# Optimization experiments

Measured on AMD Instinct MI355X. Metric: run time of the kernel, lower is better.

The kernel has to match this reference:

```python
import jax, jax.numpy as jnp
import numpy as np
import math

D_MODEL = 512
D_FF = 2048
N_HEADS = 8
D_K = 64
EPS = 1e-5


def _layernorm(x, g, b):
    mu = jnp.mean(x, axis=-1, keepdims=True)
    var = jnp.mean(jnp.square(x - mu), axis=-1, keepdims=True)
    return (x - mu) * jax.lax.rsqrt(var + EPS) * g + b


def _pos_encoding(seq_len, d_model, dtype):
    pos = jnp.arange(seq_len, dtype=jnp.float32)[:, None]                 # [S,1]
    div = jnp.exp(jnp.arange(0, d_model, 2, dtype=jnp.float32) * (-math.log(10000.0) / d_model))
    ang = pos * div                                                        # [S,D/2]
    pe = jnp.stack([jnp.sin(ang), jnp.cos(ang)], axis=-1).reshape(seq_len, d_model)
    return pe.astype(dtype)


def setup_inputs() -> dict:
    key = jax.random.key(0)
    ks = jax.random.split(key, 16)
    B, S, D, F, H, DK = 4096, 16, D_MODEL, D_FF, N_HEADS, D_K
    s = lambda fan_in: 1.0 / np.sqrt(fan_in)
    u = lambda k, shp, sc: jax.random.uniform(k, shp, jnp.float32, -sc, sc)
    return {
        "enc_inputs": jax.random.normal(ks[0], (B, S, D), jnp.float32),
        # Linear weights stored as [in, out] (torch stores [out, in])
        "wq": u(ks[1], (D, H * DK), s(D)), "bq": u(ks[2], (H * DK,), s(D)),
        "wk": u(ks[3], (D, H * DK), s(D)), "bk": u(ks[4], (H * DK,), s(D)),
        "wv": u(ks[5], (D, H * DK), s(D)), "bv": u(ks[6], (H * DK,), s(D)),
        "wo": u(ks[7], (H * DK, D), s(H * DK)), "bo": u(ks[8], (D,), s(H * DK)),
        "ln1_g": jnp.ones((D,), jnp.float32), "ln1_b": jnp.zeros((D,), jnp.float32),
        "w1": u(ks[9], (D, F), s(D)), "b1": u(ks[10], (F,), s(D)),
        "w2": u(ks[11], (F, D), s(F)), "b2": u(ks[12], (D,), s(F)),
        "ln2_g": jnp.ones((D,), jnp.float32), "ln2_b": jnp.zeros((D,), jnp.float32),
        "conv_att_w": u(ks[13], (H,), s(H)),  # Conv2d(8,1,1,bias=False) == weighted head sum
    }


def reference(enc_inputs, wq, bq, wk, bk, wv, bv, wo, bo, ln1_g, ln1_b,
              w1, b1, w2, b2, ln2_g, ln2_b, conv_att_w):
    B, S, D = enc_inputs.shape
    H, DK = N_HEADS, D_K
    # positional encoding (dropout is identity in eval)
    x = enc_inputs + _pos_encoding(S, D, enc_inputs.dtype)[None, :, :]
    # multi-head self-attention
    q = (x @ wq + bq).reshape(B, S, H, DK).transpose(0, 2, 1, 3)  # [B,H,S,DK]
    k = (x @ wk + bk).reshape(B, S, H, DK).transpose(0, 2, 1, 3)
    v = (x @ wv + bv).reshape(B, S, H, DK).transpose(0, 2, 1, 3)
    scores = jnp.einsum('bhqd,bhkd->bhqk', q, k) / np.sqrt(DK)
    attn = jax.nn.softmax(scores, axis=-1)                         # [B,H,S,S]
    ctx = jnp.einsum('bhqk,bhkd->bhqd', attn, v)
    ctx = ctx.transpose(0, 2, 1, 3).reshape(B, S, H * DK)
    y = _layernorm(ctx @ wo + bo + x, ln1_g, ln1_b)
    # position-wise FFN (conv1d kernel=1 == linear)
    h = jax.nn.relu(y @ w1 + b1)
    out = _layernorm(h @ w2 + b2 + y, ln2_g, ln2_b)
    # conv_att: Conv2d(8->1, k=1, no bias) over heads
    attn_out = jnp.einsum('h,bhqk->bqk', conv_att_w, attn)
    return out, attn_out
```

## Files before the change

### kernel.cpp

```cpp
#include <hip/hip_runtime.h>
#include <hip/hip_bf16.h>

using bf16 = __hip_bfloat16;
typedef __attribute__((ext_vector_type(8))) short bf16x8;
typedef __attribute__((ext_vector_type(4))) float f32x4;

#define MFMA_BF16_16x16x32 __builtin_amdgcn_mfma_f32_16x16x32_bf16

__device__ __forceinline__ float bits2f(short b) {
  unsigned u = ((unsigned)(unsigned short)b) << 16;
  return __uint_as_float(u);
}
__device__ __forceinline__ short f2bits(float f) {
  bf16 h = __float2bfloat16(f);
  return *reinterpret_cast<short*>(&h);
}

__device__ __forceinline__ int xcd_swz(int bid, int nwg) {
  int q = nwg >> 3;
  return (bid & 7) * q + (bid >> 3);
}

__global__ void detect_kernel(const unsigned short* __restrict__ w, int* __restrict__ flag) {
  __shared__ int bad;
  if (threadIdx.x == 0) bad = 0;
  __syncthreads();
  float m = 0.f;
#pragma unroll
  for (int j = 0; j < 4; ++j)
    m = fmaxf(m, fabsf(bits2f((short)w[threadIdx.x * 4 + j])));
  if (m > 4.0f) atomicOr(&bad, 1);
  __syncthreads();
  if (threadIdx.x == 0) *flag = bad ? 1 : 0;
}

__global__ void pe_kernel(float* __restrict__ pe) {
  int s = blockIdx.x;
  int i = threadIdx.x;
  float dv = expf((float)(2 * i) * (-9.210340371976184f / 512.0f));
  float ang = (float)s * dv;
  pe[s * 512 + 2 * i]     = sinf(ang);
  pe[s * 512 + 2 * i + 1] = cosf(ang);
}

__global__ __launch_bounds__(256) void add_pe2_kernel(const void* __restrict__ enc_bf,
                                                      const void* __restrict__ enc_f32,
                                                      const float* __restrict__ pe,
                                                      bf16* __restrict__ x,
                                                      const int* __restrict__ flag) {
  size_t i = ((size_t)blockIdx.x * 256 + threadIdx.x) * 8;
  int col  = (int)(i & 511);
  int srow = (int)((i >> 9) & 15);
  float e[8];
  if (*flag) {
    const float* ef = (const float*)enc_f32 + i;
    f32x4 a = *reinterpret_cast<const f32x4*>(ef);
    f32x4 b = *reinterpret_cast<const f32x4*>(ef + 4);
#pragma unroll
    for (int j = 0; j < 4; ++j) { e[j] = a[j]; e[4 + j] = b[j]; }
  } else {
    bf16x8 ev = *reinterpret_cast<const bf16x8*>((const bf16*)enc_bf + i);
#pragma unroll
    for (int j = 0; j < 8; ++j) e[j] = bits2f(ev[j]);
  }
  const float* pp = pe + srow * 512 + col;
  f32x4 p0 = *reinterpret_cast<const f32x4*>(pp);
  f32x4 p1 = *reinterpret_cast<const f32x4*>(pp + 4);
  bf16x8 o;
#pragma unroll
  for (int j = 0; j < 4; ++j) o[j] = f2bits(e[j] + p0[j]);
#pragma unroll
  for (int j = 0; j < 4; ++j) o[4 + j] = f2bits(e[4 + j] + p1[j]);
  *reinterpret_cast<bf16x8*>(x + i) = o;
}

__global__ __launch_bounds__(256) void transpose_cvt_kernel(const void* __restrict__ src,
                                                            unsigned short* __restrict__ dst,
                                                            int R, int C, const int* __restrict__ flag) {
  __shared__ unsigned short t[32][33];
  int bx = blockIdx.x * 32;
  int by = blockIdx.y * 32;
  int lx = threadIdx.x & 31, ly = threadIdx.x >> 5;
  if (*flag) {
    const float* s = (const float*)src;
#pragma unroll
    for (int i = 0; i < 4; ++i)
      t[ly + i * 8][lx] = (unsigned short)f2bits(s[(size_t)(by + ly + i * 8) * C + bx + lx]);
  } else {
    const unsigned short* s = (const unsigned short*)src;
#pragma unroll
    for (int i = 0; i < 4; ++i)
      t[ly + i * 8][lx] = s[(size_t)(by + ly + i * 8) * C + bx + lx];
  }
  __syncthreads();
#pragma unroll
  for (int i = 0; i < 4; ++i)
    dst[(size_t)(bx + ly + i * 8) * R + by + lx] = t[lx][ly + i * 8];
}

struct SmallSeg { const void* src; bf16* dst; int n; };
struct SmallCvtArgs { SmallSeg seg[11]; };
__global__ __launch_bounds__(256) void small_cvt_kernel(SmallCvtArgs a, const int* __restrict__ flag) {
  SmallSeg s = a.seg[blockIdx.x];
  int f = *flag;
  for (int i = threadIdx.x; i < s.n; i += 256) {
    float v = f ? ((const float*)s.src)[i] : bits2f(((const short*)s.src)[i]);
    s.dst[i] = __float2bfloat16(v);
  }
}

template <int EPI>
__global__ __launch_bounds__(256, 2)
void gemm_bt_kernel(const bf16* __restrict__ A, const bf16* __restrict__ Bt,
                    const bf16* __restrict__ bias, const bf16* res,
                    bf16* C, int M, int N, int K) {
  constexpr int BK = 32;
  __shared__ __align__(16) char lds[2][2][128 * BK * 2];
  const int nbx = N >> 7;
  const int wg = xcd_swz(blockIdx.x, gridDim.x);
  const int bx = wg % nbx;
  const int by = wg / nbx;
  const int m0 = by << 7, n0 = bx << 7;
  const int tid = threadIdx.x;
  const int lane = tid & 63, wid = tid >> 6;
  const int wm = (wid >> 1) << 6, wn = (wid & 1) << 6;
  const int lr = lane & 15, gq = lane >> 4;

  f32x4 acc[4][4] = {};

  auto stage = [&](int buf, int kt) {
#pragma unroll
    for (int c = 0; c < 2; ++c) {
      int off = c * 4096 + tid * 16;
      int row = off >> 6;
      int ch  = (off >> 4) & 3;
      const bf16* ga = A  + (size_t)(m0 + row) * K + kt * BK + ch * 8;
      const bf16* gb = Bt + (size_t)(n0 + row) * K + kt * BK + ch * 8;
      __builtin_amdgcn_global_load_lds((const __attribute__((address_space(1))) void*)ga,
          (__attribute__((address_space(3))) void*)&lds[buf][0][c * 4096 + wid * 1024], 16, 0, 0);
      __builtin_amdgcn_global_load_lds((const __attribute__((address_space(1))) void*)gb,
          (__attribute__((address_space(3))) void*)&lds[buf][1][c * 4096 + wid * 1024], 16, 0, 0);
    }
  };

  auto compute = [&](int buf) {
    const char* As = lds[buf][0];
    const char* Bs = lds[buf][1];
    bf16x8 af[4], bfr[4];
#pragma unroll
    for (int i = 0; i < 4; ++i) {
      af[i]  = *reinterpret_cast<const bf16x8*>(As + (wm + i * 16 + lr) * 64 + gq * 16);
      bfr[i] = *reinterpret_cast<const bf16x8*>(Bs + (wn + i * 16 + lr) * 64 + gq * 16);
    }
#pragma unroll
    for (int i = 0; i < 4; ++i)
#pragma unroll
      for (int j = 0; j < 4; ++j)
        acc[i][j] = MFMA_BF16_16x16x32(af[i], bfr[j], acc[i][j], 0, 0, 0);
  };

  stage(0, 0);
  __syncthreads();
  const int nk = K / BK;
  int buf = 0;
  for (int kt = 0; kt < nk; ++kt) {
    if (kt + 1 < nk) stage(buf ^ 1, kt + 1);
    compute(buf);
    __syncthreads();
    buf ^= 1;
  }

#pragma unroll
  for (int i = 0; i < 4; ++i) {
#pragma unroll
    for (int j = 0; j < 4; ++j) {
      int col = n0 + wn + j * 16 + lr;
      float bv = __bfloat162float(bias[col]);
#pragma unroll
      for (int r = 0; r < 4; ++r) {
        int row = m0 + wm + i * 16 + gq * 4 + r;
        float v = acc[i][j][r] + bv;
        if (EPI == 1) v = fmaxf(v, 0.0f);
        if (EPI == 2) v += __bfloat162float(res[(size_t)row * N + col]);
        C[(size_t)row * N + col] = __float2bfloat16(v);
      }
    }
  }
}

__global__ __launch_bounds__(256)
void attn_kernel(const bf16* __restrict__ qkv, const bf16* __restrict__ cw,
                 bf16* __restrict__ ctx, float* __restrict__ attn_out) {
  __shared__ __align__(16) unsigned short qkv_lds[16][1544];
  __shared__ __align__(16) unsigned short p_lds[4][16][16];
  __shared__ float att_lds[4][16][16];
  const int b = blockIdx.x;
  const int tid = threadIdx.x, lane = tid & 63, w = tid >> 6;
  const int lr = lane & 15, g = lane >> 4;
  const bf16* src = qkv + (size_t)b * 16 * 1536;
  for (int t = tid; t < 16 * 192; t += 256) {
    int row = t / 192, ch = t - row * 192;
    *reinterpret_cast<bf16x8*>(&qkv_lds[row][ch * 8]) =
        *reinterpret_cast<const bf16x8*>(src + (size_t)row * 1536 + ch * 8);
  }
  __syncthreads();
  float attacc[4] = {0.f, 0.f, 0.f, 0.f};

  for (int hh = 0; hh < 2; ++hh) {
    const int h = w * 2 + hh;
    const unsigned short* qp = &qkv_lds[lr][h * 64 + g * 8];
    const unsigned short* kp = qp + 512;
    bf16x8 q0 = *reinterpret_cast<const bf16x8*>(qp);
    bf16x8 q1 = *reinterpret_cast<const bf16x8*>(qp + 32);
    bf16x8 k0 = *reinterpret_cast<const bf16x8*>(kp);
    bf16x8 k1 = *reinterpret_cast<const bf16x8*>(kp + 32);
    f32x4 s = {0.f, 0.f, 0.f, 0.f};
    s = MFMA_BF16_16x16x32(q0, k0, s, 0, 0, 0);
    s = MFMA_BF16_16x16x32(q1, k1, s, 0, 0, 0);
    float wgt = __bfloat162float(cw[h]);
    float p[4];
#pragma unroll
    for (int r = 0; r < 4; ++r) {
      float sv = s[r] * 0.125f;
      float mx = sv;
#pragma unroll
      for (int mm = 1; mm < 16; mm <<= 1) mx = fmaxf(mx, __shfl_xor(mx, mm, 16));
      float e = expf(sv - mx);
      float sm = e;
#pragma unroll
      for (int mm = 1; mm < 16; mm <<= 1) sm += __shfl_xor(sm, mm, 16);
      p[r] = e / sm;
      attacc[r] += wgt * p[r];
    }
#pragma unroll
    for (int r = 0; r < 4; ++r) p_lds[w][g * 4 + r][lr] = (unsigned short)f2bits(p[r]);
    __syncthreads();
    bf16x8 pa;
#pragma unroll
    for (int j = 0; j < 8; ++j) pa[j] = 0;
    if (g < 2) pa = *reinterpret_cast<const bf16x8*>(&p_lds[w][lr][g * 8]);
#pragma unroll
    for (int n = 0; n < 4; ++n) {
      bf16x8 vb;
#pragma unroll
      for (int j = 0; j < 8; ++j) vb[j] = 0;
      if (g < 2) {
#pragma unroll
        for (int j = 0; j < 8; ++j)
          vb[j] = (short)qkv_lds[g * 8 + j][1024 + h * 64 + n * 16 + lr];
      }
      f32x4 z = {0.f, 0.f, 0.f, 0.f};
      f32x4 d = MFMA_BF16_16x16x32(pa, vb, z, 0, 0, 0);
#pragma unroll
      for (int r = 0; r < 4; ++r)
        ctx[(size_t)(b * 16 + g * 4 + r) * 512 + h * 64 + n * 16 + lr] = __float2bfloat16(d[r]);
    }
    __syncthreads();
  }
#pragma unroll
  for (int r = 0; r < 4; ++r) att_lds[w][g * 4 + r][lr] = attacc[r];
  __syncthreads();
  const int q = tid >> 4, kk = tid & 15;
  float ssum = att_lds[0][q][kk] + att_lds[1][q][kk] + att_lds[2][q][kk] + att_lds[3][q][kk];
  attn_out[(size_t)b * 256 + q * 16 + kk] = ssum;
}

template <int F32OUT>
__global__ __launch_bounds__(256, 4)
void ln_kernel(const bf16* in, const bf16* __restrict__ gw,
               const bf16* __restrict__ bw, void* out) {
  const int row = blockIdx.x * 4 + (threadIdx.x >> 6);
  const int lane = threadIdx.x & 63;
  const bf16* rp = in + (size_t)row * 512 + lane * 8;
  bf16x8 xv = *reinterpret_cast<const bf16x8*>(rp);
  float xf[8];
#pragma unroll
  for (int j = 0; j < 8; ++j) xf[j] = bits2f(xv[j]);
  float s = 0.f;
#pragma unroll
  for (int j = 0; j < 8; ++j) s += xf[j];
#pragma unroll
  for (int o = 32; o >= 1; o >>= 1) s += __shfl_xor(s, o, 64);
  float mu = s * (1.0f / 512.0f);
  float v = 0.f;
#pragma unroll
  for (int j = 0; j < 8; ++j) { float d = xf[j] - mu; v += d * d; }
#pragma unroll
  for (int o = 32; o >= 1; o >>= 1) v += __shfl_xor(v, o, 64);
  float rs = rsqrtf(v * (1.0f / 512.0f) + 1e-5f);
  bf16x8 gv = *reinterpret_cast<const bf16x8*>(gw + lane * 8);
  bf16x8 bv = *reinterpret_cast<const bf16x8*>(bw + lane * 8);
  if (F32OUT) {
    float* op = (float*)out + (size_t)row * 512 + lane * 8;
    f32x4 o0, o1;
#pragma unroll
    for (int j = 0; j < 4; ++j) {
      o0[j] = (xf[j] - mu) * rs * bits2f(gv[j]) + bits2f(bv[j]);
      o1[j] = (xf[4 + j] - mu) * rs * bits2f(gv[4 + j]) + bits2f(bv[4 + j]);
    }
    *reinterpret_cast<f32x4*>(op) = o0;
    *reinterpret_cast<f32x4*>(op + 4) = o1;
  } else {
    bf16x8 o8;
#pragma unroll
    for (int j = 0; j < 8; ++j)
      o8[j] = f2bits((xf[j] - mu) * rs * bits2f(gv[j]) + bits2f(bv[j]));
    *reinterpret_cast<bf16x8*>((bf16*)out + (size_t)row * 512 + lane * 8) = o8;
  }
}

extern "C" void kernel_launch(void* const* d_in, const int* in_sizes, int n_in,
                              void* d_out, int out_size, void* d_ws, size_t ws_size,
                              hipStream_t stream) {
  const void* enc  = d_in[0];
  const void* wq   = d_in[1];
  const void* bq   = d_in[2];
  const void* wk   = d_in[3];
  const void* bk   = d_in[4];
  const void* wv   = d_in[5];
  const void* bvv  = d_in[6];
  const void* wo   = d_in[7];
  const void* bo   = d_in[8];
  const void* ln1g = d_in[9];
  const void* ln1b = d_in[10];
  const void* w1   = d_in[11];
  const void* b1   = d_in[12];
  const void* w2   = d_in[13];
  const void* b2   = d_in[14];
  const void* ln2g = d_in[15];
  const void* ln2b = d_in[16];
  const void* cw   = d_in[17];

  float* outp     = (float*)d_out;
  float* attn_out = outp + (size_t)33554432;

  char* wsp = (char*)d_ws;
  size_t off = 0;
  auto alloc = [&](size_t bytes) {
    void* p = wsp + off;
    off = (off + bytes + 255) & ~(size_t)255;
    return p;
  };
  int*  flag  = (int*)alloc(4);
  float* pe   = (float*)alloc((size_t)16 * 512 * 4);
  bf16* wqkvT = (bf16*)alloc((size_t)1536 * 512 * 2);
  bf16* woT   = (bf16*)alloc((size_t)512 * 512 * 2);
  bf16* w1T   = (bf16*)alloc((size_t)2048 * 512 * 2);
  bf16* w2T   = (bf16*)alloc((size_t)512 * 2048 * 2);
  bf16* bqkv  = (bf16*)alloc((size_t)1536 * 2);
  bf16* bo_c  = (bf16*)alloc((size_t)512 * 2);
  bf16* b1_c  = (bf16*)alloc((size_t)2048 * 2);
  bf16* b2_c  = (bf16*)alloc((size_t)512 * 2);
  bf16* l1g_c = (bf16*)alloc((size_t)512 * 2);
  bf16* l1b_c = (bf16*)alloc((size_t)512 * 2);
  bf16* l2g_c = (bf16*)alloc((size_t)512 * 2);
  bf16* l2b_c = (bf16*)alloc((size_t)512 * 2);
  bf16* cw_c  = (bf16*)alloc((size_t)8 * 2);
  size_t fixed_bytes = off;

  int CH = 1024;
  {
    const int cands[6] = {65536, 32768, 16384, 8192, 4096, 2048};
    for (int ci = 0; ci < 6; ++ci) {
      size_t need = fixed_bytes + (size_t)cands[ci] * 6144 + (1u << 20);
      if (need <= ws_size) { CH = cands[ci]; break; }
    }
  }
  bf16* x_c   = (bf16*)alloc((size_t)CH * 512 * 2);
  bf16* ctx_c = (bf16*)alloc((size_t)CH * 512 * 2);
  bf16* share = (bf16*)alloc((size_t)CH * 2048 * 2);
  bf16* qkv = share;
  bf16* h   = share;
  bf16* y_c = ctx_c;

  detect_kernel<<<1, 256, 0, stream>>>((const unsigned short*)wq, flag);
  pe_kernel<<<16, 256, 0, stream>>>(pe);
  transpose_cvt_kernel<<<dim3(16, 16), 256, 0, stream>>>(wq, (unsigned short*)wqkvT, 512, 512, flag);
  transpose_cvt_kernel<<<dim3(16, 16), 256, 0, stream>>>(wk, (unsigned short*)(wqkvT + 512 * 512), 512, 512, flag);
  transpose_cvt_kernel<<<dim3(16, 16), 256, 0, stream>>>(wv, (unsigned short*)(wqkvT + 1024 * 512), 512, 512, flag);
  transpose_cvt_kernel<<<dim3(16, 16), 256, 0, stream>>>(wo, (unsigned short*)woT, 512, 512, flag);
  transpose_cvt_kernel<<<dim3(64, 16), 256, 0, stream>>>(w1, (unsigned short*)w1T, 512, 2048, flag);
  transpose_cvt_kernel<<<dim3(16, 64), 256, 0, stream>>>(w2, (unsigned short*)w2T, 2048, 512, flag);
  {
    SmallCvtArgs a;
    a.seg[0]  = {bq,   bqkv,        512};
    a.seg[1]  = {bk,   bqkv + 512,  512};
    a.seg[2]  = {bvv,  bqkv + 1024, 512};
    a.seg[3]  = {bo,   bo_c,        512};
    a.seg[4]  = {b1,   b1_c,       2048};
    a.seg[5]  = {b2,   b2_c,        512};
    a.seg[6]  = {ln1g, l1g_c,       512};
    a.seg[7]  = {ln1b, l1b_c,       512};
    a.seg[8]  = {ln2g, l2g_c,       512};
    a.seg[9]  = {ln2b, l2b_c,       512};
    a.seg[10] = {cw,   cw_c,          8};
    small_cvt_kernel<<<11, 256, 0, stream>>>(a, flag);
  }

  for (int r0 = 0; r0 < 65536; r0 += CH) {
    float* out_c = outp + (size_t)r0 * 512;
    float* ao_c  = attn_out + (size_t)(r0 / 16) * 256;
    add_pe2_kernel<<<CH / 4, 256, 0, stream>>>(
        (const void*)((const bf16*)enc + (size_t)r0 * 512),
        (const void*)((const float*)enc + (size_t)r0 * 512), pe, x_c, flag);
    gemm_bt_kernel<0><<<(CH / 128) * 12, 256, 0, stream>>>(x_c, wqkvT, bqkv, nullptr, qkv, CH, 1536, 512);
    attn_kernel<<<CH / 16, 256, 0, stream>>>(qkv, cw_c, ctx_c, ao_c);
    gemm_bt_kernel<2><<<(CH / 128) * 4, 256, 0, stream>>>(ctx_c, woT, bo_c, x_c, x_c, CH, 512, 512);
    ln_kernel<0><<<CH / 4, 256, 0, stream>>>(x_c, l1g_c, l1b_c, y_c);
    gemm_bt_kernel<1><<<(CH / 128) * 16, 256, 0, stream>>>(y_c, w1T, b1_c, nullptr, h, CH, 2048, 512);
    gemm_bt_kernel<2><<<(CH / 128) * 4, 256, 0, stream>>>(h, w2T, b2_c, y_c, y_c, CH, 512, 2048);
    ln_kernel<1><<<CH / 4, 256, 0, stream>>>(y_c, l2g_c, l2b_c, out_c);
  }
}
```

Baseline: 863.0 us.

## Replace GEMM with 256x256 tile, 8-wave, ping-pong scheduled MFMA kernel

```diff
diff --git a/kernel.cpp b/kernel.cpp
--- a/kernel.cpp
+++ b/kernel.cpp
@@ -109,77 +109,129 @@
   }
 }
 
+#define QUAD_MFMA(MH, NH)                                                          \
+  _Pragma("unroll") for (int mf = 0; mf < 4; ++mf)                                 \
+  _Pragma("unroll") for (int nf = 0; nf < 2; ++nf)                                 \
+  _Pragma("unroll") for (int kk = 0; kk < 2; ++kk)                                 \
+      acc[(MH) * 4 + mf][(NH) * 2 + nf] = MFMA_BF16_16x16x32(                      \
+          a[mf][kk], b[(NH) * 2 + nf][kk], acc[(MH) * 4 + mf][(NH) * 2 + nf], 0, 0, 0);
+
 template <int EPI>
-__global__ __launch_bounds__(256, 2)
-void gemm_bt_kernel(const bf16* __restrict__ A, const bf16* __restrict__ Bt,
-                    const bf16* __restrict__ bias, const bf16* res,
-                    bf16* C, int M, int N, int K) {
-  constexpr int BK = 32;
-  __shared__ __align__(16) char lds[2][2][128 * BK * 2];
-  const int nbx = N >> 7;
+__global__ __launch_bounds__(512, 2)
+void gemm8_kernel(const bf16* __restrict__ A, const bf16* __restrict__ Bt,
+                  const bf16* __restrict__ bias, const bf16* res,
+                  bf16* C, int M, int N, int K) {
+  __shared__ __align__(16) char lds[2][2][32768];
+  const int nbn = N >> 8;
   const int wg = xcd_swz(blockIdx.x, gridDim.x);
-  const int bx = wg % nbx;
-  const int by = wg / nbx;
-  const int m0 = by << 7, n0 = bx << 7;
-  const int tid = threadIdx.x;
-  const int lane = tid & 63, wid = tid >> 6;
-  const int wm = (wid >> 1) << 6, wn = (wid & 1) << 6;
+  const int bn = wg % nbn, bm = wg / nbn;
+  const int m0 = bm << 8, n0 = bn << 8;
+  const int tid = threadIdx.x, lane = tid & 63, wid = tid >> 6;
+  const int wr = wid >> 2, wc = wid & 3;
   const int lr = lane & 15, gq = lane >> 4;
-
-  f32x4 acc[4][4] = {};
-
-  auto stage = [&](int buf, int kt) {
-#pragma unroll
-    for (int c = 0; c < 2; ++c) {
-      int off = c * 4096 + tid * 16;
-      int row = off >> 6;
-      int ch  = (off >> 4) & 3;
-      const bf16* ga = A  + (size_t)(m0 + row) * K + kt * BK + ch * 8;
-      const bf16* gb = Bt + (size_t)(n0 + row) * K + kt * BK + ch * 8;
-      __builtin_amdgcn_global_load_lds((const __attribute__((address_space(1))) void*)ga,
-          (__attribute__((address_space(3))) void*)&lds[buf][0][c * 4096 + wid * 1024], 16, 0, 0);
-      __builtin_amdgcn_global_load_lds((const __attribute__((address_space(1))) void*)gb,
-          (__attribute__((address_space(3))) void*)&lds[buf][1][c * 4096 + wid * 1024], 16, 0, 0);
+  const int nt = K >> 6;
+
+  f32x4 acc[8][4] = {};
+  bf16x8 a[4][2], b[4][2];
+
+  auto stage_half = [&](int matsel, int hh, int s) {
+    const int buf = s & 1;
+    const bf16* G = matsel ? Bt : A;
+    const int base_row = (matsel ? n0 : m0) + hh * 128;
+#pragma unroll
+    for (int l = 0; l < 2; ++l) {
+      int p = l * 8192 + tid * 16;
+      int q = p ^ (((p >> 9) & 1) << 5);
+      const bf16* src = G + (size_t)(base_row + (q >> 7)) * K + s * 64 + ((q & 127) >> 1);
+      __builtin_amdgcn_global_load_lds(
+          (const __attribute__((address_space(1))) void*)src,
+          (__attribute__((address_space(3))) void*)&lds[buf][matsel][hh * 16384 + l * 8192 + wid * 1024],
+          16, 0, 0);
     }
   };
 
-  auto compute = [&](int buf) {
-    const char* As = lds[buf][0];
-    const char* Bs = lds[buf][1];
-    bf16x8 af[4], bfr[4];
-#pragma unroll
-    for (int i = 0; i < 4; ++i) {
-      af[i]  = *reinterpret_cast<const bf16x8*>(As + (wm + i * 16 + lr) * 64 + gq * 16);
-      bfr[i] = *reinterpret_cast<const bf16x8*>(Bs + (wn + i * 16 + lr) * 64 + gq * 16);
-    }
-#pragma unroll
-    for (int i = 0; i < 4; ++i)
-#pragma unroll
-      for (int j = 0; j < 4; ++j)
-        acc[i][j] = MFMA_BF16_16x16x32(af[i], bfr[j], acc[i][j], 0, 0, 0);
+  auto rd = [&](int matsel, int buf, int row, int kk) -> bf16x8 {
+    int off = row * 128 + kk * 64 + gq * 16;
+    off ^= ((off >> 9) & 1) << 5;
+    return *reinterpret_cast<const bf16x8*>(&lds[buf][matsel][off]);
   };
 
-  stage(0, 0);
-  __syncthreads();
-  const int nk = K / BK;
-  int buf = 0;
-  for (int kt = 0; kt < nk; ++kt) {
-    if (kt + 1 < nk) stage(buf ^ 1, kt + 1);
-    compute(buf);
-    __syncthreads();
-    buf ^= 1;
-  }
-
-#pragma unroll
-  for (int i = 0; i < 4; ++i) {
-#pragma unroll
-    for (int j = 0; j < 4; ++j) {
-      int col = n0 + wn + j * 16 + lr;
+  stage_half(0, 0, 0); stage_half(0, 1, 0);
+  stage_half(1, 0, 0); stage_half(1, 1, 0);
+  stage_half(1, 0, 1); stage_half(1, 1, 1);
+  asm volatile("s_waitcnt vmcnt(4)" ::: "memory");
+  __builtin_amdgcn_s_barrier();
+
+  for (int s = 0; s < nt; ++s) {
+    const int buf = s & 1;
+    const bool stA = (s + 1 < nt), stB = (s + 2 < nt);
+#pragma unroll
+    for (int mf = 0; mf < 4; ++mf)
+#pragma unroll
+      for (int kk = 0; kk < 2; ++kk)
+        a[mf][kk] = rd(0, buf, wr * 128 + mf * 16 + lr, kk);
+#pragma unroll
+    for (int nf = 0; nf < 2; ++nf)
+#pragma unroll
+      for (int kk = 0; kk < 2; ++kk)
+        b[nf][kk] = rd(1, buf, wc * 64 + nf * 16 + lr, kk);
+    if (stA) stage_half(0, 0, s + 1);
+    __builtin_amdgcn_s_barrier();
+    asm volatile("s_waitcnt lgkmcnt(0)" ::: "memory");
+    __builtin_amdgcn_sched_barrier(0);
+    __builtin_amdgcn_s_setprio(1);
+    QUAD_MFMA(0, 0)
+    __builtin_amdgcn_s_setprio(0);
+    __builtin_amdgcn_s_barrier();
+#pragma unroll
+    for (int nf = 2; nf < 4; ++nf)
+#pragma unroll
+      for (int kk = 0; kk < 2; ++kk)
+        b[nf][kk] = rd(1, buf, wc * 64 + nf * 16 + lr, kk);
+    if (stA) stage_half(0, 1, s + 1);
+    __builtin_amdgcn_s_barrier();
+    asm volatile("s_waitcnt lgkmcnt(0)" ::: "memory");
+    __builtin_amdgcn_sched_barrier(0);
+    __builtin_amdgcn_s_setprio(1);
+    QUAD_MFMA(0, 1)
+    __builtin_amdgcn_s_setprio(0);
+    __builtin_amdgcn_s_barrier();
+#pragma unroll
+    for (int mf = 0; mf < 4; ++mf)
+#pragma unroll
+      for (int kk = 0; kk < 2; ++kk)
+        a[mf][kk] = rd(0, buf, wr * 128 + 64 + mf * 16 + lr, kk);
+    if (stB) stage_half(1, 0, s + 2);
+    __builtin_amdgcn_s_barrier();
+    asm volatile("s_waitcnt lgkmcnt(0)" ::: "memory");
+    __builtin_amdgcn_sched_barrier(0);
+    __builtin_amdgcn_s_setprio(1);
+    QUAD_MFMA(1, 0)
+    __builtin_amdgcn_s_setprio(0);
+    __builtin_amdgcn_s_barrier();
+    if (stB) {
+      stage_half(1, 1, s + 2);
+      asm volatile("s_waitcnt vmcnt(4)" ::: "memory");
+    } else {
+      asm volatile("s_waitcnt vmcnt(0)" ::: "memory");
+    }
+    __builtin_amdgcn_s_barrier();
+    __builtin_amdgcn_s_setprio(1);
+    QUAD_MFMA(1, 1)
+    __builtin_amdgcn_s_setprio(0);
+    __builtin_amdgcn_s_barrier();
+  }
+
+#pragma unroll
+  for (int mf = 0; mf < 8; ++mf) {
+#pragma unroll
+    for (int nf = 0; nf < 4; ++nf) {
+      int col = n0 + wc * 64 + nf * 16 + lr;
       float bv = __bfloat162float(bias[col]);
 #pragma unroll
       for (int r = 0; r < 4; ++r) {
-        int row = m0 + wm + i * 16 + gq * 4 + r;
-        float v = acc[i][j][r] + bv;
+        int row = m0 + wr * 128 + mf * 16 + gq * 4 + r;
+        float v = acc[mf][nf][r] + bv;
         if (EPI == 1) v = fmaxf(v, 0.0f);
         if (EPI == 2) v += __bfloat162float(res[(size_t)row * N + col]);
         C[(size_t)row * N + col] = __float2bfloat16(v);
@@ -403,12 +455,12 @@
     add_pe2_kernel<<<CH / 4, 256, 0, stream>>>(
         (const void*)((const bf16*)enc + (size_t)r0 * 512),
         (const void*)((const float*)enc + (size_t)r0 * 512), pe, x_c, flag);
-    gemm_bt_kernel<0><<<(CH / 128) * 12, 256, 0, stream>>>(x_c, wqkvT, bqkv, nullptr, qkv, CH, 1536, 512);
+    gemm8_kernel<0><<<(CH / 256) * 6, 512, 0, stream>>>(x_c, wqkvT, bqkv, nullptr, qkv, CH, 1536, 512);
     attn_kernel<<<CH / 16, 256, 0, stream>>>(qkv, cw_c, ctx_c, ao_c);
-    gemm_bt_kernel<2><<<(CH / 128) * 4, 256, 0, stream>>>(ctx_c, woT, bo_c, x_c, x_c, CH, 512, 512);
+    gemm8_kernel<2><<<(CH / 256) * 2, 512, 0, stream>>>(ctx_c, woT, bo_c, x_c, x_c, CH, 512, 512);
     ln_kernel<0><<<CH / 4, 256, 0, stream>>>(x_c, l1g_c, l1b_c, y_c);
-    gemm_bt_kernel<1><<<(CH / 128) * 16, 256, 0, stream>>>(y_c, w1T, b1_c, nullptr, h, CH, 2048, 512);
-    gemm_bt_kernel<2><<<(CH / 128) * 4, 256, 0, stream>>>(h, w2T, b2_c, y_c, y_c, CH, 512, 2048);
+    gemm8_kernel<1><<<(CH / 256) * 8, 512, 0, stream>>>(y_c, w1T, b1_c, nullptr, h, CH, 2048, 512);
+    gemm8_kernel<2><<<(CH / 256) * 2, 512, 0, stream>>>(h, w2T, b2_c, y_c, y_c, CH, 512, 2048);
     ln_kernel<1><<<CH / 4, 256, 0, stream>>>(y_c, l2g_c, l2b_c, out_c);
   }
 }
```

Measured after the change: 832.5 us. -3.5%, faster.
